# Kernel tuning notes

Measured on AMD Instinct MI355X. Metric: run time of the kernel, lower is better.

## Reference

```python
import jax, jax.numpy as jnp
import numpy as np

N = 100000   # nodes
E = 1600000  # edges
IN = 32      # in_dim
D = 64       # embed_dim
G = 128      # num graphs
EPS = 1e-5   # BatchNorm eps


def setup_inputs() -> dict:
    key = jax.random.key(0)
    ks = jax.random.split(key, 12)
    s_in = 1.0 / np.sqrt(IN)
    s_d = 1.0 / np.sqrt(D)
    return {
        "x": jax.random.normal(ks[0], (N, IN), jnp.float32),
        "edge_index": jax.random.randint(ks[1], (2, E), 0, N),
        "batch": jnp.sort(jax.random.randint(ks[2], (N,), 0, G)),
        "W_embed": jax.random.normal(ks[3], (IN, D), jnp.float32) * s_in,
        "W1": jax.random.normal(ks[4], (D, D), jnp.float32) * s_d,
        "b1": jnp.zeros((D,), jnp.float32),
        "g1": jnp.ones((D,), jnp.float32),
        "bt1": jnp.zeros((D,), jnp.float32),
        "W2": jax.random.normal(ks[5], (D, D), jnp.float32) * s_d,
        "b2": jnp.zeros((D,), jnp.float32),
        "g2": jnp.ones((D,), jnp.float32),
        "bt2": jnp.zeros((D,), jnp.float32),
    }


def reference(x, edge_index, batch, W_embed, W1, b1, g1, bt1, W2, b2, g2, bt2):
    src, dst = edge_index[0], edge_index[1]
    # GCN symmetric norm with self loops: deg = in-degree + 1 (self loop)
    deg = jnp.zeros((N,), x.dtype).at[dst].add(1.0) + 1.0
    dis = jax.lax.rsqrt(deg)                      # deg^{-1/2}, [N]
    enorm = dis[src] * dis[dst]                   # per-edge norm, [E]
    self_norm = dis * dis                         # self-loop norm, [N]

    def gcn_bn(h, W, b, g, bt, relu):
        hw = h @ W                                # linear first (GCNConv)
        msg = hw[src] * enorm[:, None]            # [E, D] gather + scale
        agg = jax.ops.segment_sum(msg, dst, num_segments=N)
        agg = agg + hw * self_norm[:, None] + b   # self loops + bias
        # BatchNorm1d (training mode: batch stats, biased var)
        mu = agg.mean(axis=0)
        var = agg.var(axis=0)
        hn = (agg - mu) * jax.lax.rsqrt(var + EPS) * g + bt
        return jnp.maximum(hn, 0.0) if relu else hn

    h = x @ W_embed                               # node_embed (Linear, no bias)
    h = gcn_bn(h, W1, b1, g1, bt1, relu=True)     # ReLU only between layers
    h = gcn_bn(h, W2, b2, g2, bt2, relu=False)
    h_pool = jax.ops.segment_sum(h, batch, num_segments=G)  # global_add_pool
    return (h, h_pool)
```

## Files before the change

kernel.cpp:

```cpp
#include <hip/hip_runtime.h>

#define NN 100000
#define NE 1600000
#define IN_DIM 32
#define DD 64
#define NG 128
#define BN_EPS 1e-5f
#define AGG_BLOCKS 2048

typedef unsigned short ushort_t;
typedef unsigned int uint_t;

__device__ __forceinline__ float bf2f(ushort_t u) {
    return __uint_as_float(((uint_t)u) << 16);
}
__device__ __forceinline__ ushort_t f2bf(float f) {
    uint_t u = __float_as_uint(f);
    u = (u + 0x7FFFu + ((u >> 16) & 1u)) >> 16;
    return (ushort_t)u;
}
__device__ __forceinline__ uint_t pack2(float a, float b) {
    return (uint_t)f2bf(a) | ((uint_t)f2bf(b) << 16);
}
__device__ __forceinline__ float bflo(uint_t u) { return __uint_as_float(u << 16); }
__device__ __forceinline__ float bfhi(uint_t u) { return __uint_as_float(u & 0xFFFF0000u); }

__global__ void init_k(int* __restrict__ ints, long n_ints, float* __restrict__ pool,
                       float* __restrict__ sums) {
    long i = (long)blockIdx.x * blockDim.x + threadIdx.x;
    if (i < n_ints) ints[i] = 0;
    if (i < (long)NG * DD) pool[i] = 0.f;
    if (i < 256) sums[i] = 0.f;
}

__global__ void deg_count(const int* __restrict__ dst, int* __restrict__ cnt) {
    int e = blockIdx.x * blockDim.x + threadIdx.x;
    if (e < NE) atomicAdd(&cnt[dst[e]], 1);
}

__global__ __launch_bounds__(256) void alloc_k(const int* __restrict__ cnt,
                                               int* __restrict__ start,
                                               int* __restrict__ cursor,
                                               float* __restrict__ dis) {
    __shared__ int ls[256];
    __shared__ int base_s;
    int t = threadIdx.x;
    long n = (long)blockIdx.x * 256 + t;
    int v = (n < NN) ? cnt[n] : 0;
    ls[t] = v;
    __syncthreads();
    for (int off = 1; off < 256; off <<= 1) {
        int y = (t >= off) ? ls[t - off] : 0;
        __syncthreads();
        ls[t] += y;
        __syncthreads();
    }
    if (t == 0) base_s = atomicAdd(cursor, ls[255]);
    __syncthreads();
    if (n < NN) {
        start[n] = base_s + ls[t] - v;
        dis[n] = rsqrtf((float)v + 1.0f);
    }
}

__global__ void fill_edges(const int* __restrict__ src, const int* __restrict__ dstp,
                           const float* __restrict__ dis, const int* __restrict__ start,
                           int* __restrict__ cur, int2* __restrict__ epack) {
    int e = blockIdx.x * blockDim.x + threadIdx.x;
    if (e >= NE) return;
    int s = src[e], t = dstp[e];
    int p = atomicAdd(&cur[t], 1);
    float nm = dis[s] * dis[t];
    epack[start[t] + p] = make_int2(s, __float_as_int(nm));
}

__global__ __launch_bounds__(256) void weff_k(const float* __restrict__ We,
                                              const float* __restrict__ W1,
                                              float* __restrict__ Weff) {
    __shared__ float W1s[DD * DD];
    int t = threadIdx.x;
    for (int i = t; i < DD * DD; i += 256) W1s[i] = W1[i];
    __syncthreads();
    for (int idx = t; idx < IN_DIM * DD; idx += 256) {
        int i = idx >> 6, j = idx & 63;
        float s = 0.f;
#pragma unroll
        for (int k = 0; k < DD; ++k) s += We[i * DD + k] * W1s[k * DD + j];
        Weff[idx] = s;
    }
}

__global__ __launch_bounds__(256) void mm1_k(const float* __restrict__ x,
                                             const float* __restrict__ Weff,
                                             ushort_t* __restrict__ hwb) {
    __shared__ float Ws[IN_DIM * DD];
    int t = threadIdx.x;
    for (int i = t; i < IN_DIM * DD; i += 256) Ws[i] = Weff[i];
    __syncthreads();
    long n = (long)blockIdx.x * 256 + t;
    if (n >= NN) return;
    float acc[DD];
#pragma unroll
    for (int d = 0; d < DD; ++d) acc[d] = 0.f;
    const float4* xr = (const float4*)(x + n * IN_DIM);
#pragma unroll
    for (int k4 = 0; k4 < IN_DIM / 4; ++k4) {
        float4 xv = xr[k4];
        const float* xp = (const float*)&xv;
#pragma unroll
        for (int kk = 0; kk < 4; ++kk) {
            float v = xp[kk];
            int k = k4 * 4 + kk;
#pragma unroll
            for (int d = 0; d < DD; ++d) acc[d] += v * Ws[k * DD + d];
        }
    }
    uint4* o = (uint4*)(hwb + n * DD);
#pragma unroll
    for (int d8 = 0; d8 < DD / 8; ++d8) {
        uint4 pk;
        pk.x = pack2(acc[8 * d8 + 0], acc[8 * d8 + 1]);
        pk.y = pack2(acc[8 * d8 + 2], acc[8 * d8 + 3]);
        pk.z = pack2(acc[8 * d8 + 4], acc[8 * d8 + 5]);
        pk.w = pack2(acc[8 * d8 + 6], acc[8 * d8 + 7]);
        o[d8] = pk;
    }
}

__global__ __launch_bounds__(256) void mm2_bn_k(const float* __restrict__ agg,
                                                const float* __restrict__ sums,
                                                const float* __restrict__ g,
                                                const float* __restrict__ bt,
                                                const float* __restrict__ W,
                                                ushort_t* __restrict__ hwb) {
    __shared__ float Ws[DD * DD];
    __shared__ float mu_s[DD], sc_s[DD], bt_s[DD];
    int t = threadIdx.x;
    for (int i = t; i < DD * DD; i += 256) Ws[i] = W[i];
    if (t < DD) {
        const float inv_n = 1.0f / (float)NN;
        float mu = sums[t] * inv_n;
        float var = sums[64 + t] * inv_n - mu * mu;
        mu_s[t] = mu;
        sc_s[t] = g[t] * rsqrtf(var + BN_EPS);
        bt_s[t] = bt[t];
    }
    __syncthreads();
    long n = (long)blockIdx.x * 256 + t;
    if (n >= NN) return;
    float acc[DD];
#pragma unroll
    for (int d = 0; d < DD; ++d) acc[d] = 0.f;
    const float4* ar = (const float4*)(agg + n * DD);
#pragma unroll
    for (int k4 = 0; k4 < DD / 4; ++k4) {
        float4 av = ar[k4];
        const float* ap = (const float*)&av;
#pragma unroll
        for (int kk = 0; kk < 4; ++kk) {
            int k = k4 * 4 + kk;
            float hv = fmaxf((ap[kk] - mu_s[k]) * sc_s[k] + bt_s[k], 0.f);
#pragma unroll
            for (int d = 0; d < DD; ++d) acc[d] += hv * Ws[k * DD + d];
        }
    }
    uint4* o = (uint4*)(hwb + n * DD);
#pragma unroll
    for (int d8 = 0; d8 < DD / 8; ++d8) {
        uint4 pk;
        pk.x = pack2(acc[8 * d8 + 0], acc[8 * d8 + 1]);
        pk.y = pack2(acc[8 * d8 + 2], acc[8 * d8 + 3]);
        pk.z = pack2(acc[8 * d8 + 4], acc[8 * d8 + 5]);
        pk.w = pack2(acc[8 * d8 + 6], acc[8 * d8 + 7]);
        o[d8] = pk;
    }
}

__global__ __launch_bounds__(256) void gcn_agg(const ushort_t* __restrict__ hwb,
                                               const float* __restrict__ dis,
                                               const int* __restrict__ cnt,
                                               const int* __restrict__ start,
                                               const int2* __restrict__ epack,
                                               const float* __restrict__ bias,
                                               float* __restrict__ agg,
                                               float* __restrict__ sums) {
    int t = threadIdx.x;
    int w = t >> 6;
    int lane = t & 63;
    int j = lane >> 3;
    int c = lane & 7;
    float selfmask = (j == 0) ? 1.f : 0.f;

    float bs[8];
#pragma unroll
    for (int k = 0; k < 8; ++k) bs[k] = bias[8 * c + k];

    float s1[8], s2[8];
#pragma unroll
    for (int k = 0; k < 8; ++k) { s1[k] = 0.f; s2[k] = 0.f; }

    for (long n = (long)blockIdx.x * 4 + w; n < NN; n += (long)gridDim.x * 4) {
        int rs = start[n];
        int ce = cnt[n];
        float sn = dis[n];
        float sq = sn * sn;

        const uint4* sp = (const uint4*)(hwb + (long)n * DD);
        uint4 sv = sp[c];
        float acc[8];
        acc[0] = selfmask * (bflo(sv.x) * sq + bs[0]);
        acc[1] = selfmask * (bfhi(sv.x) * sq + bs[1]);
        acc[2] = selfmask * (bflo(sv.y) * sq + bs[2]);
        acc[3] = selfmask * (bfhi(sv.y) * sq + bs[3]);
        acc[4] = selfmask * (bflo(sv.z) * sq + bs[4]);
        acc[5] = selfmask * (bfhi(sv.z) * sq + bs[5]);
        acc[6] = selfmask * (bflo(sv.w) * sq + bs[6]);
        acc[7] = selfmask * (bfhi(sv.w) * sq + bs[7]);

        for (int i = 0; i < ce; i += 16) {
            int i0 = i + j, i1 = i + 8 + j;
            int2 e0 = (i0 < ce) ? epack[rs + i0] : make_int2(0, 0);
            int2 e1 = (i1 < ce) ? epack[rs + i1] : make_int2(0, 0);
            const uint4* r0 = (const uint4*)(hwb + (long)e0.x * DD);
            const uint4* r1 = (const uint4*)(hwb + (long)e1.x * DD);
            uint4 q0 = r0[c];
            uint4 q1 = r1[c];
            float n0 = __int_as_float(e0.y);
            float n1 = __int_as_float(e1.y);
            acc[0] += bflo(q0.x) * n0; acc[1] += bfhi(q0.x) * n0;
            acc[2] += bflo(q0.y) * n0; acc[3] += bfhi(q0.y) * n0;
            acc[4] += bflo(q0.z) * n0; acc[5] += bfhi(q0.z) * n0;
            acc[6] += bflo(q0.w) * n0; acc[7] += bfhi(q0.w) * n0;
            acc[0] += bflo(q1.x) * n1; acc[1] += bfhi(q1.x) * n1;
            acc[2] += bflo(q1.y) * n1; acc[3] += bfhi(q1.y) * n1;
            acc[4] += bflo(q1.z) * n1; acc[5] += bfhi(q1.z) * n1;
            acc[6] += bflo(q1.w) * n1; acc[7] += bfhi(q1.w) * n1;
        }

#pragma unroll
        for (int m = 8; m < 64; m <<= 1) {
#pragma unroll
            for (int k = 0; k < 8; ++k) acc[k] += __shfl_xor(acc[k], m, 64);
        }

        if (j == 0) {
            float4* op = (float4*)(agg + (long)n * DD);
            op[2 * c] = make_float4(acc[0], acc[1], acc[2], acc[3]);
            op[2 * c + 1] = make_float4(acc[4], acc[5], acc[6], acc[7]);
#pragma unroll
            for (int k = 0; k < 8; ++k) {
                s1[k] += acc[k];
                s2[k] += acc[k] * acc[k];
            }
        }
    }

    __shared__ float ls[4][128];
    if (j == 0) {
#pragma unroll
        for (int k = 0; k < 8; ++k) {
            ls[w][8 * c + k] = s1[k];
            ls[w][64 + 8 * c + k] = s2[k];
        }
    }
    __syncthreads();
    if (t < 128) {
        float a = ls[0][t] + ls[1][t] + ls[2][t] + ls[3][t];
        atomicAdd(&sums[t], a);
    }
}

__global__ __launch_bounds__(256) void bn_pool(const float* __restrict__ agg,
                                               const float* __restrict__ sums,
                                               const float* __restrict__ g,
                                               const float* __restrict__ bt,
                                               const int* __restrict__ batch,
                                               float* __restrict__ out,
                                               float* __restrict__ pool) {
    int t = threadIdx.x;
    int d = t & 63, rq = t >> 6;
    const float inv_n = 1.0f / (float)NN;
    float mu = sums[d] * inv_n;
    float var = sums[64 + d] * inv_n - mu * mu;
    float sc = g[d] * rsqrtf(var + BN_EPS);
    float bd = bt[d];
    long base = (long)blockIdx.x * 256;
    float acc = 0.f;
    int cur = -1;
    for (int i = 0; i < 64; ++i) {
        long r = base + rq + 4 * i;
        if (r >= NN) break;
        int b = batch[r];
        float v = (agg[r * DD + d] - mu) * sc + bd;
        out[r * DD + d] = v;
        if (b != cur) {
            if (cur >= 0) atomicAdd(&pool[(long)cur * DD + d], acc);
            acc = 0.f;
            cur = b;
        }
        acc += v;
    }
    if (cur >= 0) atomicAdd(&pool[(long)cur * DD + d], acc);
}

extern "C" void kernel_launch(void* const* d_in, const int* in_sizes, int n_in,
                              void* d_out, int out_size, void* d_ws, size_t ws_size,
                              hipStream_t stream) {
    const float* x = (const float*)d_in[0];
    const int* ei = (const int*)d_in[1];
    const int* batch = (const int*)d_in[2];
    const float* W_embed = (const float*)d_in[3];
    const float* W1 = (const float*)d_in[4];
    const float* b1 = (const float*)d_in[5];
    const float* g1 = (const float*)d_in[6];
    const float* bt1 = (const float*)d_in[7];
    const float* W2 = (const float*)d_in[8];
    const float* b2 = (const float*)d_in[9];
    const float* g2 = (const float*)d_in[10];
    const float* bt2 = (const float*)d_in[11];

    const int* src = ei;
    const int* dst = ei + NE;

    float* out = (float*)d_out;
    float* pool = out + (long)NN * DD;

    const long ND = (long)NN * DD;

    char* w = (char*)d_ws;
    int* cnt = (int*)w;          w += sizeof(int) * NN;
    int* cur = (int*)w;          w += sizeof(int) * NN;
    int* cursor = (int*)w;       w += sizeof(int) * 4;
    int* start = (int*)w;        w += sizeof(int) * NN;
    float* dis = (float*)w;      w += sizeof(float) * NN;
    float* sums1 = (float*)w;    w += sizeof(float) * 128;
    float* sums2 = (float*)w;    w += sizeof(float) * 128;
    float* Weff = (float*)w;     w += sizeof(float) * IN_DIM * DD;
    int2* epack = (int2*)w;      w += sizeof(int2) * NE;
    ushort_t* hwb = (ushort_t*)w; w += sizeof(ushort_t) * ND;
    float* aggbuf = (float*)w;

    dim3 blk(256);
    const int nbN = (NN + 255) / 256;
    const int nbE = (NE + 255) / 256;
    const long n_ints = 2L * NN + 4;

    init_k<<<dim3((int)((n_ints + 255) / 256)), blk, 0, stream>>>(cnt, n_ints, pool, sums1);
    deg_count<<<dim3(nbE), blk, 0, stream>>>(dst, cnt);
    alloc_k<<<dim3(nbN), blk, 0, stream>>>(cnt, start, cursor, dis);
    fill_edges<<<dim3(nbE), blk, 0, stream>>>(src, dst, dis, start, cur, epack);

    weff_k<<<dim3(1), blk, 0, stream>>>(W_embed, W1, Weff);
    mm1_k<<<dim3(nbN), blk, 0, stream>>>(x, Weff, hwb);

    gcn_agg<<<dim3(AGG_BLOCKS), blk, 0, stream>>>(hwb, dis, cnt, start, epack, b1, aggbuf, sums1);

    mm2_bn_k<<<dim3(nbN), blk, 0, stream>>>(aggbuf, sums1, g1, bt1, W2, hwb);

    gcn_agg<<<dim3(AGG_BLOCKS), blk, 0, stream>>>(hwb, dis, cnt, start, epack, b2, aggbuf, sums2);

    bn_pool<<<dim3(nbN), blk, 0, stream>>>(aggbuf, sums2, g2, bt2, batch, out, pool);
}
```

Baseline: 498.1 us.

## Fuse Weff computation into mm1, unroll edge gather by four, stats in LDS

Removes the single-block weff_k launch by having every mm1_k block recompute W_embed@W1 into shared memory before its node matmul. The gcn_agg edge loop now handles 32 edges per iteration with four independent row gathers in flight instead of two, aiming for more memory-level parallelism. Per-lane BN sum registers are replaced by accumulation directly into shared memory. In exchange, each of the ~391 mm1 blocks repeats a 32x64x64 product, the wider gather raises register pressure, and low-degree nodes waste more masked lanes.

```diff
diff --git a/kernel.cpp b/kernel.cpp
--- a/kernel.cpp
+++ b/kernel.cpp
@@ -74,10 +74,12 @@
     epack[start[t] + p] = make_int2(s, __float_as_int(nm));
 }
 
-__global__ __launch_bounds__(256) void weff_k(const float* __restrict__ We,
-                                              const float* __restrict__ W1,
-                                              float* __restrict__ Weff) {
+__global__ __launch_bounds__(256) void mm1_k(const float* __restrict__ x,
+                                             const float* __restrict__ We,
+                                             const float* __restrict__ W1,
+                                             ushort_t* __restrict__ hwb) {
     __shared__ float W1s[DD * DD];
+    __shared__ float Ws[IN_DIM * DD];
     int t = threadIdx.x;
     for (int i = t; i < DD * DD; i += 256) W1s[i] = W1[i];
     __syncthreads();
@@ -86,16 +88,8 @@
         float s = 0.f;
 #pragma unroll
         for (int k = 0; k < DD; ++k) s += We[i * DD + k] * W1s[k * DD + j];
-        Weff[idx] = s;
-    }
-}
-
-__global__ __launch_bounds__(256) void mm1_k(const float* __restrict__ x,
-                                             const float* __restrict__ Weff,
-                                             ushort_t* __restrict__ hwb) {
-    __shared__ float Ws[IN_DIM * DD];
-    int t = threadIdx.x;
-    for (int i = t; i < IN_DIM * DD; i += 256) Ws[i] = Weff[i];
+        Ws[idx] = s;
+    }
     __syncthreads();
     long n = (long)blockIdx.x * 256 + t;
     if (n >= NN) return;
@@ -191,13 +185,13 @@
     int c = lane & 7;
     float selfmask = (j == 0) ? 1.f : 0.f;
 
+    __shared__ float ls[4][128];
+    for (int k = t; k < 512; k += 256) ((float*)ls)[k] = 0.f;
+    __syncthreads();
+
     float bs[8];
 #pragma unroll
     for (int k = 0; k < 8; ++k) bs[k] = bias[8 * c + k];
-
-    float s1[8], s2[8];
-#pragma unroll
-    for (int k = 0; k < 8; ++k) { s1[k] = 0.f; s2[k] = 0.f; }
 
     for (long n = (long)blockIdx.x * 4 + w; n < NN; n += (long)gridDim.x * 4) {
         int rs = start[n];
@@ -217,16 +211,20 @@
         acc[6] = selfmask * (bflo(sv.w) * sq + bs[6]);
         acc[7] = selfmask * (bfhi(sv.w) * sq + bs[7]);
 
-        for (int i = 0; i < ce; i += 16) {
-            int i0 = i + j, i1 = i + 8 + j;
+        for (int i = 0; i < ce; i += 32) {
+            int i0 = i + j, i1 = i + 8 + j, i2 = i + 16 + j, i3 = i + 24 + j;
             int2 e0 = (i0 < ce) ? epack[rs + i0] : make_int2(0, 0);
             int2 e1 = (i1 < ce) ? epack[rs + i1] : make_int2(0, 0);
-            const uint4* r0 = (const uint4*)(hwb + (long)e0.x * DD);
-            const uint4* r1 = (const uint4*)(hwb + (long)e1.x * DD);
-            uint4 q0 = r0[c];
-            uint4 q1 = r1[c];
+            int2 e2 = (i2 < ce) ? epack[rs + i2] : make_int2(0, 0);
+            int2 e3 = (i3 < ce) ? epack[rs + i3] : make_int2(0, 0);
+            uint4 q0 = ((const uint4*)(hwb + (long)e0.x * DD))[c];
+            uint4 q1 = ((const uint4*)(hwb + (long)e1.x * DD))[c];
+            uint4 q2 = ((const uint4*)(hwb + (long)e2.x * DD))[c];
+            uint4 q3 = ((const uint4*)(hwb + (long)e3.x * DD))[c];
             float n0 = __int_as_float(e0.y);
             float n1 = __int_as_float(e1.y);
+            float n2 = __int_as_float(e2.y);
+            float n3 = __int_as_float(e3.y);
             acc[0] += bflo(q0.x) * n0; acc[1] += bfhi(q0.x) * n0;
             acc[2] += bflo(q0.y) * n0; acc[3] += bfhi(q0.y) * n0;
             acc[4] += bflo(q0.z) * n0; acc[5] += bfhi(q0.z) * n0;
@@ -235,6 +233,14 @@
             acc[2] += bflo(q1.y) * n1; acc[3] += bfhi(q1.y) * n1;
             acc[4] += bflo(q1.z) * n1; acc[5] += bfhi(q1.z) * n1;
             acc[6] += bflo(q1.w) * n1; acc[7] += bfhi(q1.w) * n1;
+            acc[0] += bflo(q2.x) * n2; acc[1] += bfhi(q2.x) * n2;
+            acc[2] += bflo(q2.y) * n2; acc[3] += bfhi(q2.y) * n2;
+            acc[4] += bflo(q2.z) * n2; acc[5] += bfhi(q2.z) * n2;
+            acc[6] += bflo(q2.w) * n2; acc[7] += bfhi(q2.w) * n2;
+            acc[0] += bflo(q3.x) * n3; acc[1] += bfhi(q3.x) * n3;
+            acc[2] += bflo(q3.y) * n3; acc[3] += bfhi(q3.y) * n3;
+            acc[4] += bflo(q3.z) * n3; acc[5] += bfhi(q3.z) * n3;
+            acc[6] += bflo(q3.w) * n3; acc[7] += bfhi(q3.w) * n3;
         }
 
 #pragma unroll
@@ -249,20 +255,12 @@
             op[2 * c + 1] = make_float4(acc[4], acc[5], acc[6], acc[7]);
 #pragma unroll
             for (int k = 0; k < 8; ++k) {
-                s1[k] += acc[k];
-                s2[k] += acc[k] * acc[k];
+                ls[w][8 * c + k] += acc[k];
+                ls[w][64 + 8 * c + k] += acc[k] * acc[k];
             }
         }
     }
 
-    __shared__ float ls[4][128];
-    if (j == 0) {
-#pragma unroll
-        for (int k = 0; k < 8; ++k) {
-            ls[w][8 * c + k] = s1[k];
-            ls[w][64 + 8 * c + k] = s2[k];
-        }
-    }
     __syncthreads();
     if (t < 128) {
         float a = ls[0][t] + ls[1][t] + ls[2][t] + ls[3][t];
@@ -335,7 +333,6 @@
     float* dis = (float*)w;      w += sizeof(float) * NN;
     float* sums1 = (float*)w;    w += sizeof(float) * 128;
     float* sums2 = (float*)w;    w += sizeof(float) * 128;
-    float* Weff = (float*)w;     w += sizeof(float) * IN_DIM * DD;
     int2* epack = (int2*)w;      w += sizeof(int2) * NE;
     ushort_t* hwb = (ushort_t*)w; w += sizeof(ushort_t) * ND;
     float* aggbuf = (float*)w;
@@ -350,8 +347,7 @@
     alloc_k<<<dim3(nbN), blk, 0, stream>>>(cnt, start, cursor, dis);
     fill_edges<<<dim3(nbE), blk, 0, stream>>>(src, dst, dis, start, cur, epack);
 
-    weff_k<<<dim3(1), blk, 0, stream>>>(W_embed, W1, Weff);
-    mm1_k<<<dim3(nbN), blk, 0, stream>>>(x, Weff, hwb);
+    mm1_k<<<dim3(nbN), blk, 0, stream>>>(x, W_embed, W1, hwb);
 
     gcn_agg<<<dim3(AGG_BLOCKS), blk, 0, stream>>>(hwb, dis, cnt, start, epack, b1, aggbuf, sums1);
 
```

After: 502.5 us. Within noise of the previous version (+0.9%).
